# Kernel tuning notes

Measured on AMD Instinct MI355X. Metric: run time of the kernel, lower is better.

Reference implementation:

```python
import jax, jax.numpy as jnp
import numpy as np


def _grid_neighbors(H, W):
    # 4-neighbor grid adjacency for the Mesh([H, W]) graph
    idx = np.arange(H * W).reshape(H, W)
    p = np.full((H + 2, W + 2), -1, dtype=np.int64)
    p[1:-1, 1:-1] = idx
    nbrs = np.stack([p[0:H, 1:W + 1], p[2:H + 2, 1:W + 1], p[1:H + 1, 0:W], p[1:H + 1, 2:W + 2]], axis=-1).reshape(H * W, 4)
    mask = (nbrs >= 0).astype(np.float32)
    return np.where(nbrs >= 0, nbrs, 0), mask, mask.sum(-1) + 1.0


def _conv(x, w, b):
    y = jax.lax.conv_general_dilated(x, w, (1, 1), 'SAME', dimension_numbers=('NCHW', 'OIHW', 'NCHW'))
    return y + b[None, :, None, None]


def _dconv(x, w1, b1, w2, b2):
    return jax.nn.relu(_conv(jax.nn.relu(_conv(x, w1, b1)), w2, b2))


def _maxpool(x):
    return jax.lax.reduce_window(x, -jnp.inf, jax.lax.max, (1, 1, 2, 2), (1, 1, 2, 2), 'VALID')


def _convT(x, w, b):
    # kernel=2, stride=2 transposed conv (non-overlapping upsample)
    y = jax.lax.conv_transpose(x, w, (2, 2), 'VALID', dimension_numbers=('NCHW', 'HWIO', 'NCHW'))
    return y + b[None, :, None, None]


def _gconv(X, W, b, nbrs, mask, deg):
    # mesh graph conv: D^-1 (A + I) X W, irregular gather over grid adjacency
    g = X[:, nbrs, :]                                          # [B, N, 4, C]
    agg = ((g * mask[None, :, :, None]).sum(2) + X) / deg[None, :, None]
    return jax.nn.relu(jnp.einsum('bnc,cd->bnd', agg, W) + b[None, None, :])


def _forward(x, d1w1, d1b1, d1w2, d1b2, d2w1, d2b1, d2w2, d2b2, md1w, md1b, md2w, md2b, mbw, mbb, mu1w, mu1b, mu2w, mu2b, u3tw, u3tb, u3w1, u3b1, u3w2, u3b2, u4tw, u4tb, u4w1, u4b1, u4w2, u4b2, ow, ob):
    b1 = _dconv(x, d1w1, d1b1, d1w2, d1b2)                     # [1,64,256,256]
    b2 = _dconv(_maxpool(b1), d2w1, d2b1, d2w2, d2b2)          # [1,128,128,128]
    fe = _maxpool(b2)                                           # [1,128,64,64]
    fe = jnp.pad(fe, ((0, 0), (0, 0), (1, 1), (1, 1)))          # pad -> 66x66
    B, C, Hm, Wm = fe.shape
    nbrs, mask, deg = _grid_neighbors(Hm, Wm)
    nbrs, mask, deg = jnp.asarray(nbrs), jnp.asarray(mask), jnp.asarray(deg)
    X = fe.reshape(B, C, Hm * Wm).transpose(0, 2, 1)            # [1, 4356, 128]
    bp1 = _gconv(X, md1w, md1b, nbrs, mask, deg)                # 256 (skip)
    bp2 = _gconv(bp1, md2w, md2b, nbrs, mask, deg)              # 512 (skip)
    Xb = _gconv(bp2, mbw, mbb, nbrs, mask, deg)                 # 1024 mesh bottleneck
    X = _gconv(Xb, mu1w, mu1b, nbrs, mask, deg) + bp2           # 512
    X = _gconv(X, mu2w, mu2b, nbrs, mask, deg) + bp1            # 256
    fe = X.transpose(0, 2, 1).reshape(B, 256, Hm, Wm)[:, :, 1:-1, 1:-1]  # unpad -> 64x64
    u3 = _convT(fe, u3tw, u3tb)                                 # [1,128,128,128]
    fe = _dconv(jnp.concatenate([b2, u3], 1), u3w1, u3b1, u3w2, u3b2)
    u4 = _convT(fe, u4tw, u4tb)                                 # [1,64,256,256]
    fe = _dconv(jnp.concatenate([b1, u4], 1), u4w1, u4b1, u4w2, u4b2)
    return _conv(fe, ow, ob)[:, 0]                              # [1,256,256]


def setup_inputs():
    ks = iter(jax.random.split(jax.random.key(0), 40))
    def W(shape, fan_in):
        return jax.random.normal(next(ks), shape, jnp.float32) * np.float32(np.sqrt(2.0 / fan_in))
    def Z(n):
        return jnp.zeros((n,), jnp.float32)
    return {
        'x': jax.random.normal(next(ks), (1, 3, 256, 256), jnp.float32),
        'd1w1': W((64, 3, 3, 3), 27), 'd1b1': Z(64), 'd1w2': W((64, 64, 3, 3), 576), 'd1b2': Z(64),
        'd2w1': W((128, 64, 3, 3), 576), 'd2b1': Z(128), 'd2w2': W((128, 128, 3, 3), 1152), 'd2b2': Z(128),
        'md1w': W((128, 256), 128), 'md1b': Z(256),
        'md2w': W((256, 512), 256), 'md2b': Z(512),
        'mbw': W((512, 1024), 512), 'mbb': Z(1024),
        'mu1w': W((1024, 512), 1024), 'mu1b': Z(512),
        'mu2w': W((512, 256), 512), 'mu2b': Z(256),
        'u3tw': W((2, 2, 256, 128), 1024), 'u3tb': Z(128),
        'u3w1': W((128, 256, 3, 3), 2304), 'u3b1': Z(128), 'u3w2': W((128, 128, 3, 3), 1152), 'u3b2': Z(128),
        'u4tw': W((2, 2, 128, 64), 512), 'u4tb': Z(64),
        'u4w1': W((64, 128, 3, 3), 1152), 'u4b1': Z(64), 'u4w2': W((64, 64, 3, 3), 576), 'u4b2': Z(64),
        'ow': W((1, 64, 3, 3), 576), 'ob': Z(1),
    }


def reference(x, d1w1, d1b1, d1w2, d1b2, d2w1, d2b1, d2w2, d2b2, md1w, md1b, md2w, md2b, mbw, mbb, mu1w, mu1b, mu2w, mu2b, u3tw, u3tb, u3w1, u3b1, u3w2, u3b2, u4tw, u4tb, u4w1, u4b1, u4w2, u4b2, ow, ob):
    return _forward(x, d1w1, d1b1, d1w2, d1b2, d2w1, d2b1, d2w2, d2b2, md1w, md1b, md2w, md2b, mbw, mbb, mu1w, mu1b, mu2w, mu2b, u3tw, u3tb, u3w1, u3b1, u3w2, u3b2, u4tw, u4tb, u4w1, u4b1, u4w2, u4b2, ow, ob)
```

## Files before the change

kernel.cpp:

```cpp
#include <hip/hip_runtime.h>
#include <cstddef>

#define TPB 256

typedef __attribute__((ext_vector_type(8))) short short8;
typedef __attribute__((ext_vector_type(4))) float f32x4;

__device__ inline unsigned short f2bf(float f) {
    unsigned int u = __builtin_bit_cast(unsigned int, f);
    u += 0x7fffu + ((u >> 16) & 1u);
    return (unsigned short)(u >> 16);
}
__device__ inline float bf2f(unsigned short h) {
    unsigned int u = ((unsigned int)h) << 16;
    return __builtin_bit_cast(float, u);
}

struct TapOffs { int o[9]; };

template<int MW, int KC>
__global__ __launch_bounds__(TPB) void k_gemm(
    const unsigned short* __restrict__ A0, const unsigned short* __restrict__ Wf,
    const float* __restrict__ bias, const unsigned short* __restrict__ resid, int RS,
    unsigned short* __restrict__ O0,
    int Cs, int AP, int Wimg, int OMS, int OP,
    int T, TapOffs toffs, int NTtot, int relu, int ct, int ctDy, int ctDx)
{
    int lane = threadIdx.x & 63, wave = threadIdx.x >> 6;
    int ml = lane & 15, kq = lane >> 4;
    int nb = blockIdx.y;

    const unsigned short* Wb = Wf;
    unsigned short* Ob = O0;
    if (ct) {
        int tp = blockIdx.z;
        Wb += (size_t)(tp * KC) * NTtot * 512;
        int dy = 1 - (tp >> 1), dx = 1 - (tp & 1);
        Ob += (size_t)dy * ctDy + (size_t)dx * ctDx;
    }
    const unsigned short* WbB = Wb + (size_t)(nb * 4) * 512 + lane * 8;

    int fy[MW], fx[MW];
    const unsigned short* Af[MW];
    #pragma unroll
    for (int f = 0; f < MW; ++f) {
        int mf = (blockIdx.x * 4 + wave) * (16 * MW) + f * 16;
        int y = mf / Wimg, x = mf - y * Wimg;
        fy[f] = y; fx[f] = x;
        Af[f] = A0 + (size_t)y * AP + (size_t)(x + ml) * Cs + kq * 8;
    }

    f32x4 acc[MW][4];
    #pragma unroll
    for (int f = 0; f < MW; ++f)
        #pragma unroll
        for (int nt = 0; nt < 4; ++nt) acc[f][nt] = (f32x4){0.f, 0.f, 0.f, 0.f};

    for (int tp = 0; tp < T; ++tp) {
        int toff = toffs.o[tp];
        const unsigned short* Wt = WbB + (size_t)(tp * KC) * NTtot * 512;
        #pragma unroll
        for (int q = 0; q < KC; ++q) {
            short8 b[4];
            #pragma unroll
            for (int nt = 0; nt < 4; ++nt)
                b[nt] = *(const short8*)(Wt + (size_t)q * NTtot * 512 + nt * 512);
            short8 a[MW];
            #pragma unroll
            for (int f = 0; f < MW; ++f)
                a[f] = *(const short8*)(Af[f] + toff + q * 32);
            #pragma unroll
            for (int f = 0; f < MW; ++f)
                #pragma unroll
                for (int nt = 0; nt < 4; ++nt)
                    acc[f][nt] = __builtin_amdgcn_mfma_f32_16x16x32_bf16(a[f], b[nt], acc[f][nt], 0, 0, 0);
        }
    }

    #pragma unroll
    for (int f = 0; f < MW; ++f) {
        unsigned short* Ot = Ob + (size_t)fy[f] * OP + (size_t)(fx[f] + kq * 4) * OMS + (size_t)nb * 64;
        int mg0 = (blockIdx.x * 4 + wave) * (16 * MW) + f * 16 + kq * 4;
        #pragma unroll
        for (int nt = 0; nt < 4; ++nt) {
            int ng = nb * 64 + nt * 16 + ml;
            float bv = bias[ng];
            #pragma unroll
            for (int r = 0; r < 4; ++r) {
                float v = acc[f][nt][r] + bv;
                if (relu) v = fmaxf(v, 0.f);
                if (resid) v += bf2f(resid[(size_t)(mg0 + r) * RS + ng]);
                Ot[(size_t)r * OMS + nt * 16 + ml] = f2bf(v);
            }
        }
    }
}

struct PackArgs {
    const float* w[15];
    int cum[16];
    int mode[15], KC[15], NT[15], K[15], N[15];
};
__global__ __launch_bounds__(TPB) void k_pack_all(
    PackArgs pa, unsigned short* __restrict__ dst, int total)
{
    int idx = blockIdx.x * TPB + threadIdx.x;
    if (idx >= total) return;
    int e = 0;
    #pragma unroll
    for (int i = 1; i < 15; ++i) e += (idx >= pa.cum[i]);
    int local = idx - pa.cum[e];
    const float* w = pa.w[e];
    int KC = pa.KC[e], NT = pa.NT[e], K = pa.K[e], N = pa.N[e], mode = pa.mode[e];

    int j = local & 7, l = (local >> 3) & 63;
    int r = local >> 9;
    int ntg = r % NT; int r2 = r / NT;
    int q = r2 % KC; int tp = r2 / KC;
    int k = q * 32 + (l >> 4) * 8 + j;
    int n = ntg * 16 + (l & 15);
    float v = 0.f;
    if (mode == 0) { int ky = tp / 3, kx = tp % 3; v = w[(size_t)(n * K + k) * 9 + ky * 3 + kx]; }
    else if (mode == 1) { v = w[(size_t)k * N + n]; }
    else if (mode == 2) { v = w[((size_t)tp * K + k) * N + n]; }
    else { if (k < 27) { int tap = k / 3, c = k % 3; int ky = tap / 3, kx = tap % 3;
                         v = w[((n * 3 + c) * 3 + ky) * 3 + kx]; } }
    dst[idx] = f2bf(v);
}

struct ZArgs { int off[10]; int cum[11]; int W2[10]; int H2[10]; int Cs[10]; };
__global__ __launch_bounds__(TPB) void k_zero_all(
    ZArgs za, unsigned short* __restrict__ W, int total)
{
    int idx = blockIdx.x * TPB + threadIdx.x;
    if (idx >= total) return;
    int e = 0;
    #pragma unroll
    for (int i = 1; i < 10; ++i) e += (idx >= za.cum[i]);
    int local = idx - za.cum[e];
    int W2 = za.W2[e], H2 = za.H2[e], Cs = za.Cs[e];
    int topbot = 2 * W2 * Cs;
    int iy, ix, c;
    if (local < topbot) {
        int row = local / (W2 * Cs); int rest = local - row * (W2 * Cs);
        iy = row ? (H2 - 1) : 0; ix = rest / Cs; c = rest - (rest / Cs) * Cs;
    } else {
        int idx2 = local - topbot;
        int per = (H2 - 2) * Cs;
        int side = idx2 / per; int rest = idx2 - side * per;
        iy = 1 + rest / Cs; ix = side ? (W2 - 1) : 0; c = rest - (rest / Cs) * Cs;
    }
    W[(size_t)za.off[e] + ((size_t)iy * W2 + ix) * Cs + c] = 0;
}

__global__ __launch_bounds__(TPB) void k_im2col(
    const float* __restrict__ x, unsigned short* __restrict__ xcol)
{
    int idx = blockIdx.x * TPB + threadIdx.x;
    if (idx >= 65536 * 32) return;
    int k = idx & 31, m = idx >> 5;
    int y = m >> 8, xx = m & 255;
    float v = 0.f;
    if (k < 27) {
        int tap = k / 3, c = k - tap * 3;
        int ty = tap / 3, tx = tap % 3;
        int yy = y + ty - 1, xp = xx + tx - 1;
        if (yy >= 0 && yy < 256 && xp >= 0 && xp < 256)
            v = x[c * 65536 + yy * 256 + xp];
    }
    xcol[idx] = f2bf(v);
}

__global__ __launch_bounds__(TPB) void k_maxpool(
    const unsigned short* __restrict__ inI, unsigned short* __restrict__ outI,
    int Wo, int C4, int CsIn, int inPitch, int CsOut, int outPitch, int total)
{
    int idx = blockIdx.x * TPB + threadIdx.x;
    if (idx >= total) return;
    int c4 = idx % C4; int p = idx / C4;
    int x = p % Wo, y = p / Wo;
    const unsigned short* ip = inI + (size_t)(2 * y) * inPitch + (size_t)(2 * x) * CsIn + c4 * 4;
    ushort4 a = *(const ushort4*)(ip);
    ushort4 b = *(const ushort4*)(ip + CsIn);
    ushort4 c = *(const ushort4*)(ip + inPitch);
    ushort4 d = *(const ushort4*)(ip + inPitch + CsIn);
    ushort4 o;
    o.x = f2bf(fmaxf(fmaxf(bf2f(a.x), bf2f(b.x)), fmaxf(bf2f(c.x), bf2f(d.x))));
    o.y = f2bf(fmaxf(fmaxf(bf2f(a.y), bf2f(b.y)), fmaxf(bf2f(c.y), bf2f(d.y))));
    o.z = f2bf(fmaxf(fmaxf(bf2f(a.z), bf2f(b.z)), fmaxf(bf2f(c.z), bf2f(d.z))));
    o.w = f2bf(fmaxf(fmaxf(bf2f(a.w), bf2f(b.w)), fmaxf(bf2f(c.w), bf2f(d.w))));
    *(ushort4*)(outI + (size_t)y * outPitch + (size_t)x * CsOut + c4 * 4) = o;
}

__global__ __launch_bounds__(TPB) void k_gagg(
    const unsigned short* __restrict__ X, unsigned short* __restrict__ agg,
    int C, int total)
{
    int idx = blockIdx.x * TPB + threadIdx.x;
    if (idx >= total) return;
    int C4 = C >> 2;
    int c4 = idx % C4; int n = idx / C4;
    int i = n / 66, j = n - i * 66;
    size_t base = (size_t)n * C + c4 * 4;
    ushort4 s = *(const ushort4*)(X + base);
    float v0 = bf2f(s.x), v1 = bf2f(s.y), v2 = bf2f(s.z), v3 = bf2f(s.w);
    float cnt = 1.f;
    if (i > 0)  { ushort4 u = *(const ushort4*)(X + base - (size_t)66 * C);
                  v0 += bf2f(u.x); v1 += bf2f(u.y); v2 += bf2f(u.z); v3 += bf2f(u.w); cnt += 1.f; }
    if (i < 65) { ushort4 u = *(const ushort4*)(X + base + (size_t)66 * C);
                  v0 += bf2f(u.x); v1 += bf2f(u.y); v2 += bf2f(u.z); v3 += bf2f(u.w); cnt += 1.f; }
    if (j > 0)  { ushort4 u = *(const ushort4*)(X + base - C);
                  v0 += bf2f(u.x); v1 += bf2f(u.y); v2 += bf2f(u.z); v3 += bf2f(u.w); cnt += 1.f; }
    if (j < 65) { ushort4 u = *(const ushort4*)(X + base + C);
                  v0 += bf2f(u.x); v1 += bf2f(u.y); v2 += bf2f(u.z); v3 += bf2f(u.w); cnt += 1.f; }
    float inv = 1.f / cnt;
    ushort4 o;
    o.x = f2bf(v0 * inv); o.y = f2bf(v1 * inv); o.z = f2bf(v2 * inv); o.w = f2bf(v3 * inv);
    *(ushort4*)(agg + base) = o;
}

__global__ __launch_bounds__(TPB) void k_outconv(
    const unsigned short* __restrict__ vI, const float* __restrict__ ow,
    const float* __restrict__ ob, float* __restrict__ out)
{
    __shared__ float wl[576];
    for (int i = threadIdx.x; i < 576; i += TPB) wl[i] = ow[i];
    __syncthreads();
    int p = blockIdx.x * TPB + threadIdx.x;
    int y = p >> 8, x = p & 255;
    float acc = ob[0];
    #pragma unroll
    for (int ky = 0; ky < 3; ++ky)
        #pragma unroll
        for (int kx = 0; kx < 3; ++kx) {
            const unsigned short* ip = vI + (size_t)((y + ky - 1) * 258 + (x + kx - 1)) * 64;
            int wb = ky * 3 + kx;
            for (int c = 0; c < 64; c += 4) {
                ushort4 uv = *(const ushort4*)(ip + c);
                acc += bf2f(uv.x) * wl[c * 9 + wb] + bf2f(uv.y) * wl[(c + 1) * 9 + wb]
                     + bf2f(uv.z) * wl[(c + 2) * 9 + wb] + bf2f(uv.w) * wl[(c + 3) * 9 + wb];
            }
        }
    out[p] = acc;
}

static inline TapOffs mk_toffs(int W2, int Cs) {
    TapOffs t;
    for (int ky = 0; ky < 3; ++ky)
        for (int kx = 0; kx < 3; ++kx)
            t.o[ky * 3 + kx] = ((ky - 1) * W2 + (kx - 1)) * Cs;
    return t;
}
static inline TapOffs zero_toffs() { TapOffs t = {}; return t; }

extern "C" void kernel_launch(void* const* d_in, const int* in_sizes, int n_in,
                              void* d_out, int out_size, void* d_ws, size_t ws_size,
                              hipStream_t stream) {
    const float* x    = (const float*)d_in[0];
    const float* d1w1 = (const float*)d_in[1];  const float* d1b1 = (const float*)d_in[2];
    const float* d1w2 = (const float*)d_in[3];  const float* d1b2 = (const float*)d_in[4];
    const float* d2w1 = (const float*)d_in[5];  const float* d2b1 = (const float*)d_in[6];
    const float* d2w2 = (const float*)d_in[7];  const float* d2b2 = (const float*)d_in[8];
    const float* md1w = (const float*)d_in[9];  const float* md1b = (const float*)d_in[10];
    const float* md2w = (const float*)d_in[11]; const float* md2b = (const float*)d_in[12];
    const float* mbw  = (const float*)d_in[13]; const float* mbb  = (const float*)d_in[14];
    const float* mu1w = (const float*)d_in[15]; const float* mu1b = (const float*)d_in[16];
    const float* mu2w = (const float*)d_in[17]; const float* mu2b = (const float*)d_in[18];
    const float* u3tw = (const float*)d_in[19]; const float* u3tb = (const float*)d_in[20];
    const float* u3w1 = (const float*)d_in[21]; const float* u3b1 = (const float*)d_in[22];
    const float* u3w2 = (const float*)d_in[23]; const float* u3b2 = (const float*)d_in[24];
    const float* u4tw = (const float*)d_in[25]; const float* u4tb = (const float*)d_in[26];
    const float* u4w1 = (const float*)d_in[27]; const float* u4b1 = (const float*)d_in[28];
    const float* u4w2 = (const float*)d_in[29]; const float* u4b2 = (const float*)d_in[30];
    const float* ow   = (const float*)d_in[31]; const float* ob   = (const float*)d_in[32];
    float* out = (float*)d_out;

    unsigned short* W = (unsigned short*)d_ws;

    const size_t XCOL = 0;
    const size_t A1   = 2097152;
    const size_t CAT4 = 6357248;
    const size_t P1   = 14877440;
    const size_t T2   = 15959040;
    const size_t CAT3 = 18122240;
    const size_t X0   = 22448640;
    const size_t BP1  = 23006208;
    const size_t BP2  = 24185856;
    const size_t XB   = 26545152;
    const size_t XC   = 31263744;
    const size_t XD   = 33623040;
    const size_t V3A  = 34802688;
    const size_t V3B  = 36965888;
    const size_t V4A  = 39129088;
    const size_t V4B  = 43389184;
    const size_t AGG  = 47649280;
    const size_t WP   = 52367872;

    const size_t a1I   = A1 + 259 * 64;
    const size_t cat4I = CAT4 + 259 * 128;
    const size_t p1I   = P1 + 131 * 64;
    const size_t t2I   = T2 + 131 * 128;
    const size_t cat3I = CAT3 + 131 * 256;
    const size_t X0I   = X0 + 67 * 128;
    const size_t XdI   = XD + 67 * 256;
    const size_t v3aI  = V3A + 131 * 128;
    const size_t v3bI  = V3B + 131 * 128;
    const size_t v4aI  = V4A + 259 * 64;
    const size_t v4bI  = V4B + 259 * 64;

    dim3 blk(TPB);
    const int BIG = 1 << 28;

    {
        ZArgs za;
        const int off[10] = {(int)A1,(int)CAT4,(int)P1,(int)T2,(int)CAT3,(int)V3A,(int)V3B,(int)V4A,(int)V4B,(int)X0};
        const int w2 [10] = {258,258,130,130,130,130,130,258,258,66};
        const int h2 [10] = {258,258,130,130,130,130,130,258,258,66};
        const int cs [10] = {64,128,64,128,256,128,128,64,64,128};
        int cum = 0;
        for (int i = 0; i < 10; ++i) {
            za.off[i]=off[i]; za.W2[i]=w2[i]; za.H2[i]=h2[i]; za.Cs[i]=cs[i];
            za.cum[i]=cum; cum += (w2[i]*h2[i] - (w2[i]-2)*(h2[i]-2))*cs[i];
        }
        za.cum[10]=cum;
        k_zero_all<<<dim3((cum + TPB - 1) / TPB), blk, 0, stream>>>(za, W, cum);
    }

    {
        PackArgs pa;
        const float* ws_[15] = {d1w1,d1w2,d2w1,d2w2,md1w,md2w,mbw,mu1w,mu2w,u3tw,u3w1,u3w2,u4tw,u4w1,u4w2};
        const int mode[15] = {3,0,0,0,1,1,1,1,1,2,0,0,2,0,0};
        const int kc [15] = {1,2,2,4,4,8,16,32,16,8,8,4,4,4,2};
        const int nt [15] = {4,4,8,8,16,32,64,32,16,8,8,8,4,4,4};
        const int kk [15] = {32,64,64,128,128,256,512,1024,512,256,256,128,128,128,64};
        const int nn [15] = {64,64,128,128,256,512,1024,512,256,128,128,128,64,64,64};
        const int tt [15] = {1,9,9,9,1,1,1,1,1,4,9,9,4,9,9};
        int cum = 0;
        for (int i = 0; i < 15; ++i) {
            pa.w[i]=ws_[i]; pa.mode[i]=mode[i]; pa.KC[i]=kc[i]; pa.NT[i]=nt[i];
            pa.K[i]=kk[i]; pa.N[i]=nn[i]; pa.cum[i]=cum;
            cum += tt[i]*kc[i]*nt[i]*512;
        }
        pa.cum[15]=cum;
        k_pack_all<<<dim3((cum + TPB - 1) / TPB), blk, 0, stream>>>(pa, W + WP, cum);
    }
    const size_t pw_d1w1=WP+0, pw_d1w2=WP+2048, pw_d2w1=WP+38912, pw_d2w2=WP+112640,
        pw_md1=WP+260096, pw_md2=WP+292864, pw_mb=WP+423936, pw_mu1=WP+948224,
        pw_mu2=WP+1472512, pw_u3t=WP+1603584, pw_u3w1=WP+1734656, pw_u3w2=WP+2029568,
        pw_u4t=WP+2177024, pw_u4w1=WP+2209792, pw_u4w2=WP+2283520;

    k_im2col<<<dim3(8192), blk, 0, stream>>>(x, W + XCOL);
    k_gemm<2,1><<<dim3(512,1), blk, 0, stream>>>(W + XCOL, W + pw_d1w1, d1b1, nullptr, 0,
        W + a1I, 32, 8192, 256, 64, 258*64, 1, zero_toffs(), 4, 1, 0,0,0);
    k_gemm<2,2><<<dim3(512,1), blk, 0, stream>>>(W + a1I, W + pw_d1w2, d1b2, nullptr, 0,
        W + cat4I, 64, 258*64, 256, 128, 258*128, 9, mk_toffs(258,64), 4, 1, 0,0,0);
    k_maxpool<<<dim3(1024), blk, 0, stream>>>(W + cat4I, W + p1I, 128, 16, 128, 258*128, 64, 130*64, 128*128*16);
    k_gemm<2,2><<<dim3(128,2), blk, 0, stream>>>(W + p1I, W + pw_d2w1, d2b1, nullptr, 0,
        W + t2I, 64, 130*64, 128, 128, 130*128, 9, mk_toffs(130,64), 8, 1, 0,0,0);
    k_gemm<2,4><<<dim3(128,2), blk, 0, stream>>>(W + t2I, W + pw_d2w2, d2b2, nullptr, 0,
        W + cat3I, 128, 130*128, 128, 256, 130*256, 9, mk_toffs(130,128), 8, 1, 0,0,0);
    k_maxpool<<<dim3(512), blk, 0, stream>>>(W + cat3I, W + X0I, 64, 32, 256, 130*256, 128, 66*128, 64*64*32);

    k_gagg<<<dim3(545), blk, 0, stream>>>(W + X0, W + AGG, 128, 4356*32);
    k_gemm<2,4><<<dim3(35,4), blk, 0, stream>>>(W + AGG, W + pw_md1, md1b, nullptr, 0,
        W + BP1, 128, 0, BIG, 256, 0, 1, zero_toffs(), 16, 1, 0,0,0);
    k_gagg<<<dim3(1089), blk, 0, stream>>>(W + BP1, W + AGG, 256, 4356*64);
    k_gemm<2,8><<<dim3(35,8), blk, 0, stream>>>(W + AGG, W + pw_md2, md2b, nullptr, 0,
        W + BP2, 256, 0, BIG, 512, 0, 1, zero_toffs(), 32, 1, 0,0,0);
    k_gagg<<<dim3(2178), blk, 0, stream>>>(W + BP2, W + AGG, 512, 4356*128);
    k_gemm<2,16><<<dim3(35,16), blk, 0, stream>>>(W + AGG, W + pw_mb, mbb, nullptr, 0,
        W + XB, 512, 0, BIG, 1024, 0, 1, zero_toffs(), 64, 1, 0,0,0);
    k_gagg<<<dim3(4356), blk, 0, stream>>>(W + XB, W + AGG, 1024, 4356*256);
    k_gemm<2,32><<<dim3(35,8), blk, 0, stream>>>(W + AGG, W + pw_mu1, mu1b, W + BP2, 512,
        W + XC, 1024, 0, BIG, 512, 0, 1, zero_toffs(), 32, 1, 0,0,0);
    k_gagg<<<dim3(2178), blk, 0, stream>>>(W + XC, W + AGG, 512, 4356*128);
    k_gemm<2,16><<<dim3(35,4), blk, 0, stream>>>(W + AGG, W + pw_mu2, mu2b, W + BP1, 256,
        W + XD, 512, 0, BIG, 256, 0, 1, zero_toffs(), 16, 1, 0,0,0);

    k_gemm<2,8><<<dim3(32,2,4), blk, 0, stream>>>(W + XdI, W + pw_u3t, u3tb, nullptr, 0,
        W + cat3I + 128, 256, 66*256, 64, 512, 2*130*256, 1, zero_toffs(), 8, 0, 1, 130*256, 256);
    k_gemm<2,8><<<dim3(128,2), blk, 0, stream>>>(W + cat3I, W + pw_u3w1, u3b1, nullptr, 0,
        W + v3aI, 256, 130*256, 128, 128, 130*128, 9, mk_toffs(130,256), 8, 1, 0,0,0);
    k_gemm<2,4><<<dim3(128,2), blk, 0, stream>>>(W + v3aI, W + pw_u3w2, u3b2, nullptr, 0,
        W + v3bI, 128, 130*128, 128, 128, 130*128, 9, mk_toffs(130,128), 8, 1, 0,0,0);

    k_gemm<2,4><<<dim3(128,1,4), blk, 0, stream>>>(W + v3bI, W + pw_u4t, u4tb, nullptr, 0,
        W + cat4I + 64, 128, 130*128, 128, 256, 2*258*128, 1, zero_toffs(), 4, 0, 1, 258*128, 128);
    k_gemm<2,4><<<dim3(512,1), blk, 0, stream>>>(W + cat4I, W + pw_u4w1, u4b1, nullptr, 0,
        W + v4aI, 128, 258*128, 256, 64, 258*64, 9, mk_toffs(258,128), 4, 1, 0,0,0);
    k_gemm<2,2><<<dim3(512,1), blk, 0, stream>>>(W + v4aI, W + pw_u4w2, u4b2, nullptr, 0,
        W + v4bI, 64, 258*64, 256, 64, 258*64, 9, mk_toffs(258,64), 4, 1, 0,0,0);

    k_outconv<<<dim3(256), blk, 0, stream>>>(W + v4bI, ow, ob, out);
}
```

Baseline: 457.7 us.

## Add LDS-tiled halo 3x3 conv kernel and widen graph GEMM M tiles

Adds a dedicated 3x3 conv kernel that loads a 6x66 pixel halo tile of one 64-channel chunk into LDS once and reuses it across all 9 taps. Weights are double-buffered per tap, and the kernel computes 4 output rows by 64 pixels by 64 channels per block with bf16 MFMA. It replaces the generic tap-offset GEMM for all seven 3x3 convolutions, cutting redundant global reads of shifted inputs. The mesh graph GEMMs also move from MW=2 to MW=4, giving fewer blocks with more rows each. The trade-offs are large LDS usage (about 73 KB) that limits occupancy, a sync after every tap, and fewer blocks for the small graph layers.

```diff
diff --git a/kernel.cpp b/kernel.cpp
--- a/kernel.cpp
+++ b/kernel.cpp
@@ -17,6 +17,104 @@
 }
 
 struct TapOffs { int o[9]; };
+
+template<int CHUNKS>
+__global__ __launch_bounds__(TPB) void k_conv3(
+    const unsigned short* __restrict__ A0, const unsigned short* __restrict__ Wf,
+    const float* __restrict__ bias, unsigned short* __restrict__ O0,
+    int AP, int tilesX, int OMS, int OP, int NTtot)
+{
+    constexpr int Cs  = CHUNKS * 64;
+    constexpr int KC2 = CHUNKS * 2;
+    __shared__ unsigned short As[6 * 66 * 72];
+    __shared__ unsigned short Bs[2][4096];
+
+    int lane = threadIdx.x & 63, wave = threadIdx.x >> 6;
+    int ml = lane & 15, kq = lane >> 4;
+    int nb = blockIdx.y;
+    int tileX = blockIdx.x % tilesX, tileY = blockIdx.x / tilesX;
+    int gx0 = tileX * 64, gy0 = tileY * 4;
+
+    f32x4 acc[4][4];
+    #pragma unroll
+    for (int mf = 0; mf < 4; ++mf)
+        #pragma unroll
+        for (int nt = 0; nt < 4; ++nt) acc[mf][nt] = (f32x4){0.f, 0.f, 0.f, 0.f};
+
+    for (int ch = 0; ch < CHUNKS; ++ch) {
+        {
+            const unsigned short* Ab = A0 + (size_t)(gy0 - 1) * AP
+                                          + (size_t)(gx0 - 1) * Cs + ch * 64;
+            for (int u = threadIdx.x; u < 6 * 66 * 8; u += TPB) {
+                int row = u / 528;
+                int rem = u - row * 528;
+                int px = rem >> 3, c16 = rem & 7;
+                int4 v = *(const int4*)(Ab + (size_t)row * AP + (size_t)px * Cs + c16 * 8);
+                *(int4*)&As[(row * 66 + px) * 72 + c16 * 8] = v;
+            }
+        }
+        {
+            const unsigned short* bsrc = Wf + ((size_t)(ch * 2) * NTtot + nb * 4) * 512;
+            for (int u = threadIdx.x; u < 512; u += TPB) {
+                int q = u >> 8, r = u & 255;
+                int4 v = *(const int4*)(bsrc + (size_t)q * NTtot * 512 + r * 8);
+                *(int4*)&Bs[0][q * 2048 + r * 8] = v;
+            }
+        }
+        __syncthreads();
+
+        for (int tap = 0; tap < 9; ++tap) {
+            if (tap < 8) {
+                const unsigned short* bsrc = Wf
+                    + ((size_t)((tap + 1) * KC2 + ch * 2) * NTtot + nb * 4) * 512;
+                unsigned short* bd = Bs[(tap + 1) & 1];
+                for (int u = threadIdx.x; u < 512; u += TPB) {
+                    int q = u >> 8, r = u & 255;
+                    int4 v = *(const int4*)(bsrc + (size_t)q * NTtot * 512 + r * 8);
+                    *(int4*)&bd[q * 2048 + r * 8] = v;
+                }
+            }
+            {
+                int ky = tap / 3, kx = tap - (tap / 3) * 3;
+                const unsigned short* Arow = &As[((wave + ky) * 66 + kx) * 72];
+                const unsigned short* Bb = &Bs[tap & 1][lane * 8];
+                #pragma unroll
+                for (int q = 0; q < 2; ++q) {
+                    short8 b[4];
+                    #pragma unroll
+                    for (int nt = 0; nt < 4; ++nt)
+                        b[nt] = *(const short8*)(Bb + q * 2048 + nt * 512);
+                    short8 a[4];
+                    #pragma unroll
+                    for (int mf = 0; mf < 4; ++mf)
+                        a[mf] = *(const short8*)(Arow + (mf * 16 + ml) * 72 + q * 32 + kq * 8);
+                    #pragma unroll
+                    for (int mf = 0; mf < 4; ++mf)
+                        #pragma unroll
+                        for (int nt = 0; nt < 4; ++nt)
+                            acc[mf][nt] = __builtin_amdgcn_mfma_f32_16x16x32_bf16(a[mf], b[nt], acc[mf][nt], 0, 0, 0);
+                }
+            }
+            __syncthreads();
+        }
+    }
+
+    int gy = gy0 + wave;
+    unsigned short* Orow = O0 + (size_t)gy * OP + (size_t)nb * 64;
+    #pragma unroll
+    for (int mf = 0; mf < 4; ++mf) {
+        int gx = gx0 + mf * 16 + kq * 4;
+        #pragma unroll
+        for (int nt = 0; nt < 4; ++nt) {
+            float bv = bias[nb * 64 + nt * 16 + ml];
+            #pragma unroll
+            for (int r = 0; r < 4; ++r) {
+                float v = fmaxf(acc[mf][nt][r] + bv, 0.f);
+                Orow[(size_t)(gx + r) * OMS + nt * 16 + ml] = f2bf(v);
+            }
+        }
+    }
+}
 
 template<int MW, int KC>
 __global__ __launch_bounds__(TPB) void k_gemm(
@@ -244,13 +342,6 @@
     out[p] = acc;
 }
 
-static inline TapOffs mk_toffs(int W2, int Cs) {
-    TapOffs t;
-    for (int ky = 0; ky < 3; ++ky)
-        for (int kx = 0; kx < 3; ++kx)
-            t.o[ky * 3 + kx] = ((ky - 1) * W2 + (kx - 1)) * Cs;
-    return t;
-}
 static inline TapOffs zero_toffs() { TapOffs t = {}; return t; }
 
 extern "C" void kernel_launch(void* const* d_in, const int* in_sizes, int n_in,
@@ -352,44 +443,44 @@
     k_im2col<<<dim3(8192), blk, 0, stream>>>(x, W + XCOL);
     k_gemm<2,1><<<dim3(512,1), blk, 0, stream>>>(W + XCOL, W + pw_d1w1, d1b1, nullptr, 0,
         W + a1I, 32, 8192, 256, 64, 258*64, 1, zero_toffs(), 4, 1, 0,0,0);
-    k_gemm<2,2><<<dim3(512,1), blk, 0, stream>>>(W + a1I, W + pw_d1w2, d1b2, nullptr, 0,
-        W + cat4I, 64, 258*64, 256, 128, 258*128, 9, mk_toffs(258,64), 4, 1, 0,0,0);
+    k_conv3<1><<<dim3(256,1), blk, 0, stream>>>(W + a1I, W + pw_d1w2, d1b2,
+        W + cat4I, 258*64, 4, 128, 258*128, 4);
     k_maxpool<<<dim3(1024), blk, 0, stream>>>(W + cat4I, W + p1I, 128, 16, 128, 258*128, 64, 130*64, 128*128*16);
-    k_gemm<2,2><<<dim3(128,2), blk, 0, stream>>>(W + p1I, W + pw_d2w1, d2b1, nullptr, 0,
-        W + t2I, 64, 130*64, 128, 128, 130*128, 9, mk_toffs(130,64), 8, 1, 0,0,0);
-    k_gemm<2,4><<<dim3(128,2), blk, 0, stream>>>(W + t2I, W + pw_d2w2, d2b2, nullptr, 0,
-        W + cat3I, 128, 130*128, 128, 256, 130*256, 9, mk_toffs(130,128), 8, 1, 0,0,0);
+    k_conv3<1><<<dim3(64,2), blk, 0, stream>>>(W + p1I, W + pw_d2w1, d2b1,
+        W + t2I, 130*64, 2, 128, 130*128, 8);
+    k_conv3<2><<<dim3(64,4), blk, 0, stream>>>(W + t2I, W + pw_d2w2, d2b2,
+        W + cat3I, 130*128, 2, 256, 130*256, 8);
     k_maxpool<<<dim3(512), blk, 0, stream>>>(W + cat3I, W + X0I, 64, 32, 256, 130*256, 128, 66*128, 64*64*32);
 
     k_gagg<<<dim3(545), blk, 0, stream>>>(W + X0, W + AGG, 128, 4356*32);
-    k_gemm<2,4><<<dim3(35,4), blk, 0, stream>>>(W + AGG, W + pw_md1, md1b, nullptr, 0,
+    k_gemm<4,4><<<dim3(18,4), blk, 0, stream>>>(W + AGG, W + pw_md1, md1b, nullptr, 0,
         W + BP1, 128, 0, BIG, 256, 0, 1, zero_toffs(), 16, 1, 0,0,0);
     k_gagg<<<dim3(1089), blk, 0, stream>>>(W + BP1, W + AGG, 256, 4356*64);
-    k_gemm<2,8><<<dim3(35,8), blk, 0, stream>>>(W + AGG, W + pw_md2, md2b, nullptr, 0,
+    k_gemm<4,8><<<dim3(18,8), blk, 0, stream>>>(W + AGG, W + pw_md2, md2b, nullptr, 0,
         W + BP2, 256, 0, BIG, 512, 0, 1, zero_toffs(), 32, 1, 0,0,0);
     k_gagg<<<dim3(2178), blk, 0, stream>>>(W + BP2, W + AGG, 512, 4356*128);
-    k_gemm<2,16><<<dim3(35,16), blk, 0, stream>>>(W + AGG, W + pw_mb, mbb, nullptr, 0,
+    k_gemm<4,16><<<dim3(18,16), blk, 0, stream>>>(W + AGG, W + pw_mb, mbb, nullptr, 0,
         W + XB, 512, 0, BIG, 1024, 0, 1, zero_toffs(), 64, 1, 0,0,0);
     k_gagg<<<dim3(4356), blk, 0, stream>>>(W + XB, W + AGG, 1024, 4356*256);
-    k_gemm<2,32><<<dim3(35,8), blk, 0, stream>>>(W + AGG, W + pw_mu1, mu1b, W + BP2, 512,
+    k_gemm<4,32><<<dim3(18,8), blk, 0, stream>>>(W + AGG, W + pw_mu1, mu1b, W + BP2, 512,
         W + XC, 1024, 0, BIG, 512, 0, 1, zero_toffs(), 32, 1, 0,0,0);
     k_gagg<<<dim3(2178), blk, 0, stream>>>(W + XC, W + AGG, 512, 4356*128);
-    k_gemm<2,16><<<dim3(35,4), blk, 0, stream>>>(W + AGG, W + pw_mu2, mu2b, W + BP1, 256,
+    k_gemm<4,16><<<dim3(18,4), blk, 0, stream>>>(W + AGG, W + pw_mu2, mu2b, W + BP1, 256,
         W + XD, 512, 0, BIG, 256, 0, 1, zero_toffs(), 16, 1, 0,0,0);
 
     k_gemm<2,8><<<dim3(32,2,4), blk, 0, stream>>>(W + XdI, W + pw_u3t, u3tb, nullptr, 0,
         W + cat3I + 128, 256, 66*256, 64, 512, 2*130*256, 1, zero_toffs(), 8, 0, 1, 130*256, 256);
-    k_gemm<2,8><<<dim3(128,2), blk, 0, stream>>>(W + cat3I, W + pw_u3w1, u3b1, nullptr, 0,
-        W + v3aI, 256, 130*256, 128, 128, 130*128, 9, mk_toffs(130,256), 8, 1, 0,0,0);
-    k_gemm<2,4><<<dim3(128,2), blk, 0, stream>>>(W + v3aI, W + pw_u3w2, u3b2, nullptr, 0,
-        W + v3bI, 128, 130*128, 128, 128, 130*128, 9, mk_toffs(130,128), 8, 1, 0,0,0);
+    k_conv3<4><<<dim3(64,2), blk, 0, stream>>>(W + cat3I, W + pw_u3w1, u3b1,
+        W + v3aI, 130*256, 2, 128, 130*128, 8);
+    k_conv3<2><<<dim3(64,2), blk, 0, stream>>>(W + v3aI, W + pw_u3w2, u3b2,
+        W + v3bI, 130*128, 2, 128, 130*128, 8);
 
     k_gemm<2,4><<<dim3(128,1,4), blk, 0, stream>>>(W + v3bI, W + pw_u4t, u4tb, nullptr, 0,
         W + cat4I + 64, 128, 130*128, 128, 256, 2*258*128, 1, zero_toffs(), 4, 0, 1, 258*128, 128);
-    k_gemm<2,4><<<dim3(512,1), blk, 0, stream>>>(W + cat4I, W + pw_u4w1, u4b1, nullptr, 0,
-        W + v4aI, 128, 258*128, 256, 64, 258*64, 9, mk_toffs(258,128), 4, 1, 0,0,0);
-    k_gemm<2,2><<<dim3(512,1), blk, 0, stream>>>(W + v4aI, W + pw_u4w2, u4b2, nullptr, 0,
-        W + v4bI, 64, 258*64, 256, 64, 258*64, 9, mk_toffs(258,64), 4, 1, 0,0,0);
+    k_conv3<2><<<dim3(256,1), blk, 0, stream>>>(W + cat4I, W + pw_u4w1, u4b1,
+        W + v4aI, 258*128, 4, 64, 258*64, 4);
+    k_conv3<1><<<dim3(256,1), blk, 0, stream>>>(W + v4aI, W + pw_u4w2, u4b2,
+        W + v4bI, 258*64, 4, 64, 258*64, 4);
 
     k_outconv<<<dim3(256), blk, 0, stream>>>(W + v4bI, ow, ob, out);
 }
```

Result: slower. 513.9 us (+12.3%).
